# Kernel optimization log

Measured on AMD Instinct MI355X. Metric: run time of the kernel, lower is better.

Reference implementation:

```python
import jax, jax.numpy as jnp
import numpy as np

N_NODES = 500000
N_EDGES = 8000000
REPR_DIM = 32
TEMPO_DIM = 8
N_CLUSTERS = 5
NUM_NEG = 3
BATCH_SIZE = 100000  # multiple of NUM_NEG+2 = 5


def setup_inputs() -> dict:
    key = jax.random.key(0)
    ks = jax.random.split(key, 24)
    s = 0.05
    inp = {
        'x': jax.random.normal(ks[0], (N_NODES, 32), jnp.float32),
        'weight': jax.random.uniform(ks[1], (N_EDGES,), jnp.float32),
        # positional (repr) GraphSAGE params
        'e_w1l': jax.random.normal(ks[2], (32, REPR_DIM)) * s,
        'e_b1l': jax.random.normal(ks[3], (REPR_DIM,)) * s,
        'e_w1r': jax.random.normal(ks[4], (32 + REPR_DIM, REPR_DIM)) * s,
        'e_b1r': jax.random.normal(ks[5], (REPR_DIM,)) * s,
        'e_w2l': jax.random.normal(ks[6], (REPR_DIM, REPR_DIM)) * s,
        'e_b2l': jax.random.normal(ks[7], (REPR_DIM,)) * s,
        'e_w2r': jax.random.normal(ks[8], (2 * REPR_DIM, REPR_DIM)) * s,
        'e_b2r': jax.random.normal(ks[9], (REPR_DIM,)) * s,
        # temporal GraphSAGE params
        't_w1l': jax.random.normal(ks[10], (32, TEMPO_DIM)) * s,
        't_b1l': jax.random.normal(ks[11], (TEMPO_DIM,)) * s,
        't_w1r': jax.random.normal(ks[12], (32 + TEMPO_DIM, TEMPO_DIM)) * s,
        't_b1r': jax.random.normal(ks[13], (TEMPO_DIM,)) * s,
        't_w2l': jax.random.normal(ks[14], (TEMPO_DIM, TEMPO_DIM)) * s,
        't_b2l': jax.random.normal(ks[15], (TEMPO_DIM,)) * s,
        't_w2r': jax.random.normal(ks[16], (2 * TEMPO_DIM, TEMPO_DIM)) * s,
        't_b2r': jax.random.normal(ks[17], (TEMPO_DIM,)) * s,
        # centroid embeddings
        'cent': jax.random.normal(ks[18], (N_CLUSTERS, REPR_DIM)),
        'cent_t': jax.random.normal(ks[19], (N_CLUSTERS, TEMPO_DIM)),
        'edge_index': jax.random.randint(ks[20], (2, N_EDGES), 0, N_NODES, jnp.int32),
        'batch_size': BATCH_SIZE,
    }
    return inp


def _pinsage_layer(x, src, dst, w, Wl, bl, Wr, br):
    # z_n = relu(lin_l(x)); agg = weighted-mean of z_n over incoming edges
    n = x.shape[0]
    z = jax.nn.relu(x @ Wl + bl)                               # [N, d]
    agg_w = jax.ops.segment_sum(w, dst, num_segments=n) + 1.0  # [N]
    gathered = z[src] * w[:, None]                             # [E, d]
    agg = jax.ops.segment_sum(gathered, dst, num_segments=n) / agg_w[:, None]
    return jax.nn.relu(jnp.concatenate([x, agg], axis=1) @ Wr + br)


def _sage_module(x, src, dst, w, w1l, b1l, w1r, b1r, w2l, b2l, w2r, b2r, bs):
    h = _pinsage_layer(x, src, dst, w, w1l, b1l, w1r, b1r)
    h = jax.nn.relu(h)  # redundant (already relu'd) but matches source
    h = _pinsage_layer(h, src, dst, w, w2l, b2l, w2r, b2r)
    return h[:bs]


def reference(x, weight, e_w1l, e_b1l, e_w1r, e_b1r, e_w2l, e_b2l, e_w2r, e_b2r,
              t_w1l, t_b1l, t_w1r, t_b1r, t_w2l, t_b2l, t_w2r, t_b2r,
              cent, cent_t, edge_index, batch_size):
    src, dst = edge_index[0], edge_index[1]
    emb_posi = _sage_module(x, src, dst, weight, e_w1l, e_b1l, e_w1r, e_b1r,
                            e_w2l, e_b2l, e_w2r, e_b2r, batch_size)
    emb_temp = _sage_module(x, src, dst, weight, t_w1l, t_b1l, t_w1r, t_b1r,
                            t_w2l, t_b2l, t_w2r, t_b2r, batch_size)
    k = NUM_NEG + 2
    b = batch_size // k
    z = jnp.concatenate([emb_posi.reshape(b, k, REPR_DIM),
                         emb_temp.reshape(b, k, TEMPO_DIM)], axis=2)  # [B,5,40]
    ctr, pos, neg = z[:, 0], z[:, 1], z[:, 2:]
    pos_d = jnp.sum(ctr * pos, axis=-1)                                # [B]
    neg_d = jnp.max(jnp.einsum('bd,bkd->bk', ctr, neg), axis=1)        # [B]
    mm_loss = jnp.mean(jnp.maximum(neg_d - pos_d + 1.0, 0.0))
    # soft centroid assignment loss (optimize_comms=True path)
    C = jnp.concatenate([cent, cent_t], axis=1)                        # [K,40]
    q_ctr = jax.nn.softmax(ctr @ C.T, axis=-1)                         # [B,K]
    q_pos = jax.nn.softmax(pos @ C.T, axis=-1)                         # [B,K]
    q_neg = jax.nn.softmax(neg @ C.T, axis=-1)                         # [B,3,K]
    c_pos_d = jnp.sum(q_ctr * q_pos, axis=-1)
    c_neg_d = jnp.max(jnp.einsum('bc,bkc->bk', q_ctr, q_neg), axis=1)
    c_mm_loss = jnp.mean(jnp.maximum(c_neg_d - c_pos_d + 1.0, 0.0))
    q = jnp.concatenate([q_ctr[:, None], q_pos[:, None], q_neg], axis=1).reshape(-1, N_CLUSTERS)
    ne = jnp.mean(jnp.sum(q * jnp.log(q + 1e-20), axis=-1))  # negative entropy regularizer
    return mm_loss + c_mm_loss + ne * 0.01
```

## Files before the change

### kernel.cpp

```cpp
#include <hip/hip_runtime.h>

#define BS 100000
#define BQ 20000
#define NWG 512
#define CB  1024
#define NCMAX 512
#define CAP 17408

typedef unsigned long long ull;

__device__ __forceinline__ float relu_(float v) { return fmaxf(v, 0.0f); }

__device__ __forceinline__ unsigned enc12(float f) {
    unsigned u = __float_as_uint(f);
    if (u < 0x38000000u) return 0u;
    unsigned r = u - 0x38000000u;
    unsigned b = (r + 0x7FFFu + ((r >> 16) & 1u)) >> 16;
    return (b > 0xFFFu) ? 0xFFFu : b;
}
__device__ __forceinline__ float dec12(unsigned b) {
    return __uint_as_float((b << 16) + 0x38000000u);
}


__global__ __launch_bounds__(1024) void hist_kernel(
    const int* __restrict__ dst, int E, int NC, int per, int* __restrict__ hist2D)
{
    __shared__ int lc[NCMAX];
    int t = threadIdx.x, g = blockIdx.x;
    for (int i = t; i < NC; i += 1024) lc[i] = 0;
    __syncthreads();
    int lo = g * per, hi = min(lo + per, E);
    if (lo < hi) {
        int nq = (hi - lo) >> 2;
        const int4* dst4 = (const int4*)(dst + lo);
        for (int q = t; q < nq; q += 1024) {
            int4 d = dst4[q];
            atomicAdd(&lc[d.x >> 10], 1);
            atomicAdd(&lc[d.y >> 10], 1);
            atomicAdd(&lc[d.z >> 10], 1);
            atomicAdd(&lc[d.w >> 10], 1);
        }
        for (int i = lo + (nq << 2) + t; i < hi; i += 1024)
            atomicAdd(&lc[dst[i] >> 10], 1);
    }
    __syncthreads();
    for (int b = t; b < NC; b += 1024) hist2D[(size_t)b * NWG + g] = lc[b];
}

__global__ __launch_bounds__(256) void reduce_kernel(
    const int* __restrict__ hist2D, int* __restrict__ bucketTot)
{
    __shared__ int s[256];
    int b = blockIdx.x, t = threadIdx.x;
    int sum = 0;
    for (int g = t; g < NWG; g += 256) sum += hist2D[(size_t)b * NWG + g];
    s[t] = sum;
    __syncthreads();
    for (int d = 128; d > 0; d >>= 1) {
        if (t < d) s[t] += s[t + d];
        __syncthreads();
    }
    if (t == 0) bucketTot[b] = s[0];
}

__global__ __launch_bounds__(512) void scanTot_kernel(
    const int* __restrict__ bucketTot, int NC, int* __restrict__ bucketBase)
{
    __shared__ int s[512];
    int t = threadIdx.x;
    int v = (t < NC) ? bucketTot[t] : 0;
    s[t] = v;
    __syncthreads();
    for (int d = 1; d < 512; d <<= 1) {
        int x = (t >= d) ? s[t - d] : 0;
        __syncthreads();
        s[t] += x;
        __syncthreads();
    }
    if (t < NC) bucketBase[t] = s[t] - v;
}

__global__ __launch_bounds__(NWG) void scanB_kernel(
    const int* __restrict__ hist2D, const int* __restrict__ bucketBase,
    int* __restrict__ wgbase)
{
    __shared__ int s[NWG];
    int b = blockIdx.x, g = threadIdx.x;
    int v = hist2D[(size_t)b * NWG + g];
    s[g] = v;
    __syncthreads();
    for (int d = 1; d < NWG; d <<= 1) {
        int x = (g >= d) ? s[g - d] : 0;
        __syncthreads();
        s[g] += x;
        __syncthreads();
    }
    wgbase[(size_t)b * NWG + g] = bucketBase[b] + s[g] - v;
}

__device__ __forceinline__ void fillA_one(int d, int s, float wv,
    int* cur, ull* __restrict__ tmp)
{
    int b = d >> 10;
    int pos = atomicAdd(&cur[b], 1);
    ull rec = (ull)__float_as_uint(wv)
            | ((ull)(unsigned int)s << 32)
            | ((ull)(unsigned int)(d & (CB - 1)) << 51);
    tmp[pos] = rec;
}

__global__ __launch_bounds__(1024) void fillA_kernel(
    const int* __restrict__ src, const int* __restrict__ dst,
    const float* __restrict__ w, int E, int NC, int per,
    const int* __restrict__ wgbase, ull* __restrict__ tmp)
{
    __shared__ int cur[NCMAX];
    int t = threadIdx.x, g = blockIdx.x;
    for (int i = t; i < NC; i += 1024) cur[i] = wgbase[(size_t)i * NWG + g];
    __syncthreads();
    int lo = g * per, hi = min(lo + per, E);
    if (lo >= hi) return;
    int nq = (hi - lo) >> 2;
    const int4* src4 = (const int4*)(src + lo);
    const int4* dst4 = (const int4*)(dst + lo);
    const float4* w4 = (const float4*)(w + lo);
    for (int q = t; q < nq; q += 1024) {
        int4 d = dst4[q];
        int4 s = src4[q];
        float4 wv = w4[q];
        fillA_one(d.x, s.x, wv.x, cur, tmp);
        fillA_one(d.y, s.y, wv.y, cur, tmp);
        fillA_one(d.z, s.z, wv.z, cur, tmp);
        fillA_one(d.w, s.w, wv.w, cur, tmp);
    }
    for (int i = lo + (nq << 2) + t; i < hi; i += 1024)
        fillA_one(dst[i], src[i], w[i], cur, tmp);
}

__global__ __launch_bounds__(1024) void fillA2B_kernel(
    const ull* __restrict__ tmp, const int* __restrict__ wgbase,
    int NC, int N, int E,
    unsigned* __restrict__ csr, int* __restrict__ offsets)
{
    __shared__ int cnt[CB];
    __shared__ int ssum[1024];
    extern __shared__ unsigned recs[];
    int b = blockIdx.x, t = threadIdx.x;
    int lo = wgbase[(size_t)b * NWG];
    int hi = (b == NC - 1) ? E : wgbase[(size_t)(b + 1) * NWG];
    int M = hi - lo;

    cnt[t] = 0;
    __syncthreads();
    {
        int k = t;
        for (; k + 1024 < M; k += 2048) {
            ull r0 = tmp[lo + k];
            ull r1 = tmp[lo + k + 1024];
            atomicAdd(&cnt[(int)(r0 >> 51)], 1);
            atomicAdd(&cnt[(int)(r1 >> 51)], 1);
        }
        if (k < M) atomicAdd(&cnt[(int)(tmp[lo + k] >> 51)], 1);
    }
    __syncthreads();

    int v = cnt[t];
    ssum[t] = v;
    __syncthreads();
    for (int d = 1; d < 1024; d <<= 1) {
        int x = (t >= d) ? ssum[t - d] : 0;
        __syncthreads();
        ssum[t] += x;
        __syncthreads();
    }
    int excl = ssum[t] - v;

    int node = b * CB + t;
    if (node < N) offsets[node] = lo + excl;
    if (b == NC - 1 && t == 0) offsets[N] = E;
    __syncthreads();
    cnt[t] = excl;
    __syncthreads();

    if (M <= CAP) {
        for (int e = lo + t; e < hi; e += 1024) {
            ull rec = tmp[e];
            int dl = (int)(rec >> 51);
            int pos = atomicAdd(&cnt[dl], 1);
            float w = __uint_as_float((unsigned int)(rec & 0xFFFFFFFFull));
            unsigned wq = (unsigned)fmaf(w, 8191.0f, 0.5f);
            unsigned sidx = (unsigned)((rec >> 32) & 0x7FFFFull);
            recs[pos] = (sidx << 13) | wq;
        }
        __syncthreads();
        for (int i = t; i < M; i += 1024)
            csr[lo + i] = recs[i];
    } else {
        for (int e = lo + t; e < hi; e += 1024) {
            ull rec = tmp[e];
            int dl = (int)(rec >> 51);
            int pos = atomicAdd(&cnt[dl], 1);
            float w = __uint_as_float((unsigned int)(rec & 0xFFFFFFFFull));
            unsigned wq = (unsigned)fmaf(w, 8191.0f, 0.5f);
            unsigned sidx = (unsigned)((rec >> 32) & 0x7FFFFull);
            csr[lo + pos] = (sidx << 13) | wq;
        }
    }
}

__global__ __launch_bounds__(256) void z1_kernel(
    const float* __restrict__ in,
    const float* __restrict__ we, const float* __restrict__ be,
    const float* __restrict__ wt, const float* __restrict__ bt,
    unsigned* __restrict__ zq, int n)
{
    __shared__ float sWe[32 * 32];
    __shared__ float sWt[32 * 8];
    __shared__ float sBe[32];
    __shared__ float sBt[8];
    for (int i = threadIdx.x; i < 32 * 32; i += 256) sWe[i] = we[i];
    for (int i = threadIdx.x; i < 32 * 8; i += 256) sWt[i] = wt[i];
    if (threadIdx.x < 32) sBe[threadIdx.x] = be[threadIdx.x];
    if (threadIdx.x < 8)  sBt[threadIdx.x] = bt[threadIdx.x];
    __syncthreads();

    int node = blockIdx.x * 256 + threadIdx.x;
    if (node >= n) return;

    float row[32];
    {
        const float4* rp = (const float4*)(in + (size_t)node * 32);
        #pragma unroll
        for (int q = 0; q < 8; q++) {
            float4 v = rp[q];
            row[4*q] = v.x; row[4*q+1] = v.y; row[4*q+2] = v.z; row[4*q+3] = v.w;
        }
    }

    float o[40];
    #pragma unroll
    for (int j = 0; j < 32; j++) o[j] = sBe[j];
    #pragma unroll
    for (int i = 0; i < 32; i++) {
        float v = row[i];
        #pragma unroll
        for (int j = 0; j < 32; j++) o[j] = fmaf(v, sWe[i * 32 + j], o[j]);
    }
    #pragma unroll
    for (int j = 0; j < 8; j++) o[32 + j] = sBt[j];
    #pragma unroll
    for (int i = 0; i < 32; i++) {
        float v = row[i];
        #pragma unroll
        for (int j = 0; j < 8; j++) o[32 + j] = fmaf(v, sWt[i * 8 + j], o[32 + j]);
    }

    unsigned b[40];
    #pragma unroll
    for (int i = 0; i < 40; i++) b[i] = enc12(relu_(o[i]));
    unsigned wd[16];
    #pragma unroll
    for (int k = 0; k < 5; k++) {
        wd[3*k+0] = b[8*k+0] | (b[8*k+1] << 12) | (b[8*k+2] << 24);
        wd[3*k+1] = (b[8*k+2] >> 8) | (b[8*k+3] << 4) | (b[8*k+4] << 16) | (b[8*k+5] << 28);
        wd[3*k+2] = (b[8*k+5] >> 4) | (b[8*k+6] << 8) | (b[8*k+7] << 20);
    }
    wd[15] = 0;
    uint4* zv = (uint4*)(zq + (size_t)node * 16);
    #pragma unroll
    for (int q = 0; q < 4; q++)
        zv[q] = make_uint4(wd[4*q], wd[4*q+1], wd[4*q+2], wd[4*q+3]);
}

__device__ __forceinline__ void acc_edge(float* acc, float w,
    const uint4& A, const uint4& B, const uint4& C, const uint4& D)
{
    unsigned wds[15] = {A.x, A.y, A.z, A.w, B.x, B.y, B.z, B.w,
                        C.x, C.y, C.z, C.w, D.x, D.y, D.z};
    #pragma unroll
    for (int k = 0; k < 5; k++) {
        unsigned xw = wds[3*k+0], yw = wds[3*k+1], zw = wds[3*k+2];
        acc[8*k+0] = fmaf(w, dec12(xw & 0xFFFu),                       acc[8*k+0]);
        acc[8*k+1] = fmaf(w, dec12((xw >> 12) & 0xFFFu),               acc[8*k+1]);
        acc[8*k+2] = fmaf(w, dec12(((xw >> 24) | (yw << 8)) & 0xFFFu), acc[8*k+2]);
        acc[8*k+3] = fmaf(w, dec12((yw >> 4) & 0xFFFu),                acc[8*k+3]);
        acc[8*k+4] = fmaf(w, dec12((yw >> 16) & 0xFFFu),               acc[8*k+4]);
        acc[8*k+5] = fmaf(w, dec12(((yw >> 28) | (zw << 4)) & 0xFFFu), acc[8*k+5]);
        acc[8*k+6] = fmaf(w, dec12((zw >> 8) & 0xFFFu),                acc[8*k+6]);
        acc[8*k+7] = fmaf(w, dec12((zw >> 20) & 0xFFFu),               acc[8*k+7]);
    }
}

template <int RW, int TIN, int TOFF, bool EMITZ>
__global__ __launch_bounds__(256) void fin_kernel(
    const float* __restrict__ in,
    const unsigned* __restrict__ zq,
    const int* __restrict__ offsets,
    const unsigned* __restrict__ csr,
    const float* __restrict__ wre, const float* __restrict__ bre,
    const float* __restrict__ wrt, const float* __restrict__ brt,
    const float* __restrict__ w2e, const float* __restrict__ b2e,
    const float* __restrict__ w2t, const float* __restrict__ b2t,
    float* __restrict__ outbuf, int nOut,
    unsigned* __restrict__ zq2,
    int n)
{
    __shared__ float sWe[64 * 32];
    __shared__ float sWt[(TIN + 8) * 8];
    __shared__ float sBe[32];
    __shared__ float sBt[8];
    __shared__ float sW2e[32 * 32];
    __shared__ float sW2t[8 * 8];
    __shared__ float sB2e[32];
    __shared__ float sB2t[8];
    for (int i = threadIdx.x; i < 64 * 32; i += 256) sWe[i] = wre[i];
    for (int i = threadIdx.x; i < (TIN + 8) * 8; i += 256) sWt[i] = wrt[i];
    if (threadIdx.x < 32) sBe[threadIdx.x] = bre[threadIdx.x];
    if (threadIdx.x < 8)  sBt[threadIdx.x] = brt[threadIdx.x];
    if (EMITZ) {
        for (int i = threadIdx.x; i < 32 * 32; i += 256) sW2e[i] = w2e[i];
        for (int i = threadIdx.x; i < 8 * 8; i += 256) sW2t[i] = w2t[i];
        if (threadIdx.x < 32) sB2e[threadIdx.x] = b2e[threadIdx.x];
        if (threadIdx.x < 8)  sB2t[threadIdx.x] = b2t[threadIdx.x];
    }
    __syncthreads();

    int node = blockIdx.x * 256 + threadIdx.x;
    if (node >= n) return;

    float acc[40];
    #pragma unroll
    for (int j = 0; j < 40; j++) acc[j] = 0.0f;
    float wsum = 1.0f;

    const float DW = 1.0f / 8191.0f;
    int e0 = offsets[node];
    int e1 = offsets[node + 1];
    int e = e0;
    for (; e + 2 <= e1; e += 2) {
        unsigned pk0 = csr[e];
        unsigned pk1 = csr[e + 1];
        const uint4* p0 = (const uint4*)(zq + (size_t)(pk0 >> 13) * 16);
        const uint4* p1 = (const uint4*)(zq + (size_t)(pk1 >> 13) * 16);
        uint4 A0 = p0[0], B0 = p0[1], C0 = p0[2], D0 = p0[3];
        uint4 A1 = p1[0], B1 = p1[1], C1 = p1[2], D1 = p1[3];
        float w0 = (float)(pk0 & 8191u) * DW;
        float w1 = (float)(pk1 & 8191u) * DW;
        acc_edge(acc, w0, A0, B0, C0, D0);
        acc_edge(acc, w1, A1, B1, C1, D1);
        wsum += w0;
        wsum += w1;
    }
    if (e < e1) {
        unsigned pk = csr[e];
        const uint4* zp = (const uint4*)(zq + (size_t)(pk >> 13) * 16);
        uint4 A = zp[0], B = zp[1], C = zp[2], D = zp[3];
        float w = (float)(pk & 8191u) * DW;
        acc_edge(acc, w, A, B, C, D);
        wsum += w;
    }
    float inv = 1.0f / wsum;
    #pragma unroll
    for (int j = 0; j < 40; j++) acc[j] *= inv;

    float row[RW];
    {
        const float4* rp = (const float4*)(in + (size_t)node * RW);
        #pragma unroll
        for (int q = 0; q < RW / 4; q++) {
            float4 v = rp[q];
            row[4*q] = v.x; row[4*q+1] = v.y; row[4*q+2] = v.z; row[4*q+3] = v.w;
        }
    }

    float h[40];

    {
        float o[32];
        #pragma unroll
        for (int j = 0; j < 32; j++) o[j] = sBe[j];
        #pragma unroll
        for (int i = 0; i < 32; i++) {
            float v = row[i];
            #pragma unroll
            for (int j = 0; j < 32; j++) o[j] = fmaf(v, sWe[i * 32 + j], o[j]);
        }
        #pragma unroll
        for (int i = 0; i < 32; i++) {
            float v = acc[i];
            #pragma unroll
            for (int j = 0; j < 32; j++) o[j] = fmaf(v, sWe[(32 + i) * 32 + j], o[j]);
        }
        #pragma unroll
        for (int j = 0; j < 32; j++) h[j] = relu_(o[j]);
    }
    {
        float ot[8];
        #pragma unroll
        for (int j = 0; j < 8; j++) ot[j] = sBt[j];
        #pragma unroll
        for (int i = 0; i < TIN; i++) {
            float v = row[TOFF + i];
            #pragma unroll
            for (int j = 0; j < 8; j++) ot[j] = fmaf(v, sWt[i * 8 + j], ot[j]);
        }
        #pragma unroll
        for (int i = 0; i < 8; i++) {
            float v = acc[32 + i];
            #pragma unroll
            for (int j = 0; j < 8; j++) ot[j] = fmaf(v, sWt[(TIN + i) * 8 + j], ot[j]);
        }
        #pragma unroll
        for (int j = 0; j < 8; j++) h[32 + j] = relu_(ot[j]);
    }

    if (node < nOut) {
        float4* ov = (float4*)(outbuf + (size_t)node * 40);
        #pragma unroll
        for (int q = 0; q < 10; q++)
            ov[q] = make_float4(h[4*q], h[4*q+1], h[4*q+2], h[4*q+3]);
    }

    if (EMITZ) {
        float z2[40];
        #pragma unroll
        for (int j = 0; j < 32; j++) z2[j] = sB2e[j];
        #pragma unroll
        for (int i = 0; i < 32; i++) {
            float v = h[i];
            #pragma unroll
            for (int j = 0; j < 32; j++) z2[j] = fmaf(v, sW2e[i * 32 + j], z2[j]);
        }
        #pragma unroll
        for (int j = 0; j < 8; j++) z2[32 + j] = sB2t[j];
        #pragma unroll
        for (int i = 0; i < 8; i++) {
            float v = h[32 + i];
            #pragma unroll
            for (int j = 0; j < 8; j++) z2[32 + j] = fmaf(v, sW2t[i * 8 + j], z2[32 + j]);
        }
        unsigned b[40];
        #pragma unroll
        for (int i = 0; i < 40; i++) b[i] = enc12(relu_(z2[i]));
        unsigned wd[16];
        #pragma unroll
        for (int k = 0; k < 5; k++) {
            wd[3*k+0] = b[8*k+0] | (b[8*k+1] << 12) | (b[8*k+2] << 24);
            wd[3*k+1] = (b[8*k+2] >> 8) | (b[8*k+3] << 4) | (b[8*k+4] << 16) | (b[8*k+5] << 28);
            wd[3*k+2] = (b[8*k+5] >> 4) | (b[8*k+6] << 8) | (b[8*k+7] << 20);
        }
        wd[15] = 0;
        uint4* zv = (uint4*)(zq2 + (size_t)node * 16);
        #pragma unroll
        for (int q = 0; q < 4; q++)
            zv[q] = make_uint4(wd[4*q], wd[4*q+1], wd[4*q+2], wd[4*q+3]);
    }
}


__device__ __forceinline__ void load40(const float* p, float* r) {
    const float4* v = (const float4*)p;
    #pragma unroll
    for (int q = 0; q < 10; q++) {
        float4 t = v[q];
        r[4*q] = t.x; r[4*q+1] = t.y; r[4*q+2] = t.z; r[4*q+3] = t.w;
    }
}

__device__ __forceinline__ float dot40(const float* a, const float* b) {
    float s = 0.0f;
    #pragma unroll
    for (int d = 0; d < 40; d++) s = fmaf(a[d], b[d], s);
    return s;
}

__device__ __forceinline__ void softmax5(const float l[5], float q[5]) {
    float m = l[0];
    #pragma unroll
    for (int c = 1; c < 5; c++) m = fmaxf(m, l[c]);
    float s = 0.0f;
    #pragma unroll
    for (int c = 0; c < 5; c++) { q[c] = expf(l[c] - m); s += q[c]; }
    float inv = 1.0f / s;
    #pragma unroll
    for (int c = 0; c < 5; c++) q[c] *= inv;
}

__device__ __forceinline__ float ent5(const float q[5]) {
    float e = 0.0f;
    #pragma unroll
    for (int c = 0; c < 5; c++) e += q[c] * logf(q[c] + 1e-20f);
    return e;
}

__device__ __forceinline__ float dot5(const float* a, const float* b) {
    float s = 0.0f;
    #pragma unroll
    for (int c = 0; c < 5; c++) s += a[c] * b[c];
    return s;
}

__global__ __launch_bounds__(256) void loss_kernel(
    const float* __restrict__ emb,
    const float* __restrict__ cent,
    const float* __restrict__ cent_t,
    float* __restrict__ out)
{
    __shared__ float sC[5 * 40];
    for (int i = threadIdx.x; i < 200; i += 256) {
        int c = i / 40, d = i % 40;
        sC[i] = (d < 32) ? cent[c * 32 + d] : cent_t[c * 8 + (d - 32)];
    }
    __syncthreads();

    int i = blockIdx.x * 256 + threadIdx.x;
    float contrib = 0.0f;
    if (i < BQ) {
        const float* base = emb + (size_t)i * 200;

        float ctr[40];
        load40(base, ctr);
        float l[5];
        #pragma unroll
        for (int c = 0; c < 5; c++) l[c] = dot40(ctr, sC + c * 40);
        float qc[5];
        softmax5(l, qc);
        float ent = ent5(qc);

        float rowv[40];
        load40(base + 40, rowv);
        float pd = dot40(ctr, rowv);
        #pragma unroll
        for (int c = 0; c < 5; c++) l[c] = dot40(rowv, sC + c * 40);
        float qp[5];
        softmax5(l, qp);
        float cpd = dot5(qc, qp);
        ent += ent5(qp);

        float nd = -1e30f, cnd = -1e30f;
        #pragma unroll
        for (int k = 0; k < 3; k++) {
            load40(base + (2 + k) * 40, rowv);
            nd = fmaxf(nd, dot40(ctr, rowv));
            #pragma unroll
            for (int c = 0; c < 5; c++) l[c] = dot40(rowv, sC + c * 40);
            float qn[5];
            softmax5(l, qn);
            cnd = fmaxf(cnd, dot5(qc, qn));
            ent += ent5(qn);
        }

        float mm  = fmaxf(nd - pd + 1.0f, 0.0f);
        float cmm = fmaxf(cnd - cpd + 1.0f, 0.0f);
        contrib = (mm + cmm) * (1.0f / (float)BQ) + 0.01f * (1.0f / (float)BS) * ent;
    }

    #pragma unroll
    for (int off = 32; off > 0; off >>= 1) contrib += __shfl_down(contrib, off);
    if ((threadIdx.x & 63) == 0) atomicAdd(out, contrib);
}


extern "C" void kernel_launch(void* const* d_in, const int* in_sizes, int n_in,
                              void* d_out, int out_size, void* d_ws, size_t ws_size,
                              hipStream_t stream) {
    const float* x      = (const float*)d_in[0];
    const float* weight = (const float*)d_in[1];
    const float* e_w1l  = (const float*)d_in[2];
    const float* e_b1l  = (const float*)d_in[3];
    const float* e_w1r  = (const float*)d_in[4];
    const float* e_b1r  = (const float*)d_in[5];
    const float* e_w2l  = (const float*)d_in[6];
    const float* e_b2l  = (const float*)d_in[7];
    const float* e_w2r  = (const float*)d_in[8];
    const float* e_b2r  = (const float*)d_in[9];
    const float* t_w1l  = (const float*)d_in[10];
    const float* t_b1l  = (const float*)d_in[11];
    const float* t_w1r  = (const float*)d_in[12];
    const float* t_b1r  = (const float*)d_in[13];
    const float* t_w2l  = (const float*)d_in[14];
    const float* t_b2l  = (const float*)d_in[15];
    const float* t_w2r  = (const float*)d_in[16];
    const float* t_b2r  = (const float*)d_in[17];
    const float* cent   = (const float*)d_in[18];
    const float* cent_t = (const float*)d_in[19];
    const int*   eidx   = (const int*)d_in[20];

    const int E = in_sizes[20] / 2;
    const int N = in_sizes[0] / 32;
    const int* srcI = eidx;
    const int* dstI = eidx + E;
    float* out = (float*)d_out;

    const int NC = (N + CB - 1) / CB;
    const int per = (((E + NWG - 1) / NWG) + 3) & ~3;

    char* p = (char*)d_ws;
    auto alloc = [&](size_t bytes) -> char* {
        char* r = p;
        p += (bytes + 255) & ~(size_t)255;
        return r;
    };
    char* regionA = alloc((size_t)E * 8);
    ull*  tmp     = (ull*)regionA;
    unsigned* zq1 = (unsigned*)regionA;
    unsigned* zq2 = (unsigned*)alloc((size_t)N * 64);
    float* hcat   = (float*)alloc((size_t)BS * 40 * 4);
    float* emb    = (float*)alloc((size_t)BS * 40 * 4);
    unsigned* csr = (unsigned*)alloc((size_t)E * 4);
    int*   offsets= (int*)alloc((size_t)(N + 1) * 4);
    int*   hist2D = (int*)alloc((size_t)NC * NWG * 4);
    int*   wgbase = (int*)alloc((size_t)NC * NWG * 4);
    int*   bucketTot  = (int*)alloc((size_t)NC * 4);
    int*   bucketBase = (int*)alloc((size_t)NC * 4);
    (void)ws_size;

    hipMemsetAsync(d_out, 0, sizeof(float), stream);

    hist_kernel<<<NWG, 1024, 0, stream>>>(dstI, E, NC, per, hist2D);
    reduce_kernel<<<NC, 256, 0, stream>>>(hist2D, bucketTot);
    scanTot_kernel<<<1, 512, 0, stream>>>(bucketTot, NC, bucketBase);
    scanB_kernel<<<NC, NWG, 0, stream>>>(hist2D, bucketBase, wgbase);
    fillA_kernel<<<NWG, 1024, 0, stream>>>(srcI, dstI, weight, E, NC, per, wgbase, tmp);
    fillA2B_kernel<<<NC, 1024, (size_t)CAP * 4, stream>>>(tmp, wgbase, NC, N, E, csr, offsets);

    const int nb = (N + 255) / 256;
    z1_kernel<<<nb, 256, 0, stream>>>(x, e_w1l, e_b1l, t_w1l, t_b1l, zq1, N);
    fin_kernel<32, 32, 0, true><<<nb, 256, 0, stream>>>(
        x, zq1, offsets, csr,
        e_w1r, e_b1r, t_w1r, t_b1r,
        e_w2l, e_b2l, t_w2l, t_b2l,
        hcat, BS, zq2, N);
    const int nb2 = (BS + 255) / 256;
    fin_kernel<40, 8, 32, false><<<nb2, 256, 0, stream>>>(
        hcat, zq2, offsets, csr,
        e_w2r, e_b2r, t_w2r, t_b2r,
        nullptr, nullptr, nullptr, nullptr,
        emb, BS, nullptr, BS);

    loss_kernel<<<(BQ + 255) / 256, 256, 0, stream>>>(emb, cent, cent_t, out);
}
```

Measured before the change: 506.5 us.

## Stage fillA scatter writes in LDS ring buffers and flush full cache lines

The bucket-scatter pass now stages records in a per-bucket shared-memory ring and flushes completed 8-record (64-byte) lines to global memory as whole lines, instead of writing each 8-byte record to a random address. To keep those lines aligned, each workgroup's per-bucket segment is padded to a multiple of 8. Records carry a valid bit, and the later CSR pass skips padding entries. Two separate bucket scans are kept, one padded and one actual, so CSR offsets stay compact. The trade-off is extra block-wide barriers and flush loops per edge step, a slightly larger temporary buffer, and padded reads in the second pass.

After: 462.6 us. 8.7% less time.

```diff
diff --git a/kernel.cpp b/kernel.cpp
--- a/kernel.cpp
+++ b/kernel.cpp
@@ -6,6 +6,7 @@
 #define CB  1024
 #define NCMAX 512
 #define CAP 17408
+#define RING_D 16
 
 typedef unsigned long long ull;
 
@@ -49,27 +50,34 @@
 }
 
 __global__ __launch_bounds__(256) void reduce_kernel(
-    const int* __restrict__ hist2D, int* __restrict__ bucketTot)
-{
-    __shared__ int s[256];
+    const int* __restrict__ hist2D, int* __restrict__ bucketTotPad,
+    int* __restrict__ bucketTotAct)
+{
+    __shared__ int sp[256];
+    __shared__ int sa[256];
     int b = blockIdx.x, t = threadIdx.x;
-    int sum = 0;
-    for (int g = t; g < NWG; g += 256) sum += hist2D[(size_t)b * NWG + g];
-    s[t] = sum;
+    int sumP = 0, sumA = 0;
+    for (int g = t; g < NWG; g += 256) {
+        int c = hist2D[(size_t)b * NWG + g];
+        sumA += c;
+        sumP += (c + 7) & ~7;
+    }
+    sp[t] = sumP; sa[t] = sumA;
     __syncthreads();
     for (int d = 128; d > 0; d >>= 1) {
-        if (t < d) s[t] += s[t + d];
-        __syncthreads();
-    }
-    if (t == 0) bucketTot[b] = s[0];
+        if (t < d) { sp[t] += sp[t + d]; sa[t] += sa[t + d]; }
+        __syncthreads();
+    }
+    if (t == 0) { bucketTotPad[b] = sp[0]; bucketTotAct[b] = sa[0]; }
 }
 
 __global__ __launch_bounds__(512) void scanTot_kernel(
-    const int* __restrict__ bucketTot, int NC, int* __restrict__ bucketBase)
+    const int* __restrict__ bucketTotPad, const int* __restrict__ bucketTotAct,
+    int NC, int* __restrict__ bucketBasePad, int* __restrict__ bucketBaseAct)
 {
     __shared__ int s[512];
     int t = threadIdx.x;
-    int v = (t < NC) ? bucketTot[t] : 0;
+    int v = (t < NC) ? bucketTotPad[t] : 0;
     s[t] = v;
     __syncthreads();
     for (int d = 1; d < 512; d <<= 1) {
@@ -78,16 +86,28 @@
         s[t] += x;
         __syncthreads();
     }
-    if (t < NC) bucketBase[t] = s[t] - v;
+    if (t < NC) bucketBasePad[t] = s[t] - v;
+    if (t == NC - 1) bucketBasePad[NC] = s[t];
+    __syncthreads();
+    int va = (t < NC) ? bucketTotAct[t] : 0;
+    s[t] = va;
+    __syncthreads();
+    for (int d = 1; d < 512; d <<= 1) {
+        int x = (t >= d) ? s[t - d] : 0;
+        __syncthreads();
+        s[t] += x;
+        __syncthreads();
+    }
+    if (t < NC) bucketBaseAct[t] = s[t] - va;
 }
 
 __global__ __launch_bounds__(NWG) void scanB_kernel(
-    const int* __restrict__ hist2D, const int* __restrict__ bucketBase,
+    const int* __restrict__ hist2D, const int* __restrict__ bucketBasePad,
     int* __restrict__ wgbase)
 {
     __shared__ int s[NWG];
     int b = blockIdx.x, g = threadIdx.x;
-    int v = hist2D[(size_t)b * NWG + g];
+    int v = (hist2D[(size_t)b * NWG + g] + 7) & ~7;
     s[g] = v;
     __syncthreads();
     for (int d = 1; d < NWG; d <<= 1) {
@@ -96,18 +116,7 @@
         s[g] += x;
         __syncthreads();
     }
-    wgbase[(size_t)b * NWG + g] = bucketBase[b] + s[g] - v;
-}
-
-__device__ __forceinline__ void fillA_one(int d, int s, float wv,
-    int* cur, ull* __restrict__ tmp)
-{
-    int b = d >> 10;
-    int pos = atomicAdd(&cur[b], 1);
-    ull rec = (ull)__float_as_uint(wv)
-            | ((ull)(unsigned int)s << 32)
-            | ((ull)(unsigned int)(d & (CB - 1)) << 51);
-    tmp[pos] = rec;
+    wgbase[(size_t)b * NWG + g] = bucketBasePad[b] + s[g] - v;
 }
 
 __global__ __launch_bounds__(1024) void fillA_kernel(
@@ -115,31 +124,122 @@
     const float* __restrict__ w, int E, int NC, int per,
     const int* __restrict__ wgbase, ull* __restrict__ tmp)
 {
+    extern __shared__ ull ring[];
     __shared__ int cur[NCMAX];
+    __shared__ int flq[NCMAX];
+    __shared__ unsigned vmask[NCMAX];
     int t = threadIdx.x, g = blockIdx.x;
-    for (int i = t; i < NC; i += 1024) cur[i] = wgbase[(size_t)i * NWG + g];
-    __syncthreads();
+    for (int i = t; i < NC; i += 1024) {
+        int base = wgbase[(size_t)i * NWG + g];
+        cur[i] = base;
+        flq[i] = base >> 3;
+        vmask[i] = 0u;
+    }
+    __syncthreads();
+
     int lo = g * per, hi = min(lo + per, E);
-    if (lo >= hi) return;
-    int nq = (hi - lo) >> 2;
-    const int4* src4 = (const int4*)(src + lo);
-    const int4* dst4 = (const int4*)(dst + lo);
-    const float4* w4 = (const float4*)(w + lo);
-    for (int q = t; q < nq; q += 1024) {
-        int4 d = dst4[q];
-        int4 s = src4[q];
-        float4 wv = w4[q];
-        fillA_one(d.x, s.x, wv.x, cur, tmp);
-        fillA_one(d.y, s.y, wv.y, cur, tmp);
-        fillA_one(d.z, s.z, wv.z, cur, tmp);
-        fillA_one(d.w, s.w, wv.w, cur, tmp);
-    }
-    for (int i = lo + (nq << 2) + t; i < hi; i += 1024)
-        fillA_one(dst[i], src[i], w[i], cur, tmp);
+    int groups = (per + 4095) >> 12;
+    for (int gi = 0; gi < groups; gi++) {
+        int eb = lo + (gi << 12) + (t << 2);
+        int4 d4 = make_int4(0, 0, 0, 0), s4 = make_int4(0, 0, 0, 0);
+        float4 w4 = make_float4(0, 0, 0, 0);
+        if (eb + 4 <= hi) {
+            d4 = *(const int4*)(dst + eb);
+            s4 = *(const int4*)(src + eb);
+            w4 = *(const float4*)(w + eb);
+        } else if (eb < hi) {
+            int m = hi - eb;
+            if (m > 0) { d4.x = dst[eb];     s4.x = src[eb];     w4.x = w[eb]; }
+            if (m > 1) { d4.y = dst[eb + 1]; s4.y = src[eb + 1]; w4.y = w[eb + 1]; }
+            if (m > 2) { d4.z = dst[eb + 2]; s4.z = src[eb + 2]; w4.z = w[eb + 2]; }
+        }
+        #pragma unroll
+        for (int k = 0; k < 4; k++) {
+            if (eb + k < hi) {
+                int d = (k == 0) ? d4.x : (k == 1) ? d4.y : (k == 2) ? d4.z : d4.w;
+                int s = (k == 0) ? s4.x : (k == 1) ? s4.y : (k == 2) ? s4.z : s4.w;
+                float wv = (k == 0) ? w4.x : (k == 1) ? w4.y : (k == 2) ? w4.z : w4.w;
+                int b = d >> 10;
+                ull rec = (1ull << 63)
+                        | ((ull)(unsigned)(d & (CB - 1)) << 51)
+                        | ((ull)(unsigned)s << 32)
+                        | (ull)__float_as_uint(wv);
+                int pos = atomicAdd(&cur[b], 1);
+                if ((pos >> 3) < flq[b] + 2) {
+                    int slot = pos & 15;
+                    ring[b * RING_D + slot] = rec;
+                    atomicOr(&vmask[b], 1u << slot);
+                } else {
+                    tmp[pos] = rec;
+                }
+            }
+            __syncthreads();
+            if (t < NC) {
+                int bb = t;
+                int endL = cur[bb] >> 3;
+                int L = flq[bb];
+                unsigned vm = vmask[bb];
+                while (L < endL) {
+                    int half = (L & 1) << 3;
+                    unsigned m8 = (vm >> half) & 0xFFu;
+                    ull* dp = tmp + ((size_t)L << 3);
+                    const ull* rp = ring + bb * RING_D + half;
+                    if (m8 == 0xFFu) {
+                        uint4* d16 = (uint4*)dp;
+                        const uint4* r16 = (const uint4*)rp;
+                        d16[0] = r16[0]; d16[1] = r16[1];
+                        d16[2] = r16[2]; d16[3] = r16[3];
+                    } else if (m8) {
+                        #pragma unroll
+                        for (int j = 0; j < 8; j++)
+                            if (m8 & (1u << j)) dp[j] = rp[j];
+                    }
+                    vm &= ~(0xFFu << half);
+                    L++;
+                }
+                vmask[bb] = vm;
+                flq[bb] = L;
+            }
+            __syncthreads();
+        }
+    }
+
+    if (t < NC) {
+        int bb = t;
+        int c = cur[bb];
+        int padded = (c + 7) & ~7;
+        unsigned vm = vmask[bb];
+        for (int p = c; p < padded; p++) {
+            int slot = p & 15;
+            ring[bb * RING_D + slot] = 0ull;
+            vm |= 1u << slot;
+        }
+        int endL = padded >> 3;
+        int L = flq[bb];
+        while (L < endL) {
+            int half = (L & 1) << 3;
+            unsigned m8 = (vm >> half) & 0xFFu;
+            ull* dp = tmp + ((size_t)L << 3);
+            const ull* rp = ring + bb * RING_D + half;
+            if (m8 == 0xFFu) {
+                uint4* d16 = (uint4*)dp;
+                const uint4* r16 = (const uint4*)rp;
+                d16[0] = r16[0]; d16[1] = r16[1];
+                d16[2] = r16[2]; d16[3] = r16[3];
+            } else if (m8) {
+                #pragma unroll
+                for (int j = 0; j < 8; j++)
+                    if (m8 & (1u << j)) dp[j] = rp[j];
+            }
+            vm &= ~(0xFFu << half);
+            L++;
+        }
+    }
 }
 
 __global__ __launch_bounds__(1024) void fillA2B_kernel(
     const ull* __restrict__ tmp, const int* __restrict__ wgbase,
+    const int* __restrict__ bucketBasePad, const int* __restrict__ bucketBaseAct,
     int NC, int N, int E,
     unsigned* __restrict__ csr, int* __restrict__ offsets)
 {
@@ -148,20 +248,14 @@
     extern __shared__ unsigned recs[];
     int b = blockIdx.x, t = threadIdx.x;
     int lo = wgbase[(size_t)b * NWG];
-    int hi = (b == NC - 1) ? E : wgbase[(size_t)(b + 1) * NWG];
-    int M = hi - lo;
+    int hi = (b == NC - 1) ? bucketBasePad[NC] : wgbase[(size_t)(b + 1) * NWG];
+    int actLo = bucketBaseAct[b];
 
     cnt[t] = 0;
     __syncthreads();
-    {
-        int k = t;
-        for (; k + 1024 < M; k += 2048) {
-            ull r0 = tmp[lo + k];
-            ull r1 = tmp[lo + k + 1024];
-            atomicAdd(&cnt[(int)(r0 >> 51)], 1);
-            atomicAdd(&cnt[(int)(r1 >> 51)], 1);
-        }
-        if (k < M) atomicAdd(&cnt[(int)(tmp[lo + k] >> 51)], 1);
+    for (int e = lo + t; e < hi; e += 1024) {
+        ull rec = tmp[e];
+        if (rec >> 63) atomicAdd(&cnt[(int)((rec >> 51) & (CB - 1))], 1);
     }
     __syncthreads();
 
@@ -175,18 +269,20 @@
         __syncthreads();
     }
     int excl = ssum[t] - v;
+    int Mact = ssum[1023];
 
     int node = b * CB + t;
-    if (node < N) offsets[node] = lo + excl;
+    if (node < N) offsets[node] = actLo + excl;
     if (b == NC - 1 && t == 0) offsets[N] = E;
     __syncthreads();
     cnt[t] = excl;
     __syncthreads();
 
-    if (M <= CAP) {
+    if (Mact <= CAP) {
         for (int e = lo + t; e < hi; e += 1024) {
             ull rec = tmp[e];
-            int dl = (int)(rec >> 51);
+            if (!(rec >> 63)) continue;
+            int dl = (int)((rec >> 51) & (CB - 1));
             int pos = atomicAdd(&cnt[dl], 1);
             float w = __uint_as_float((unsigned int)(rec & 0xFFFFFFFFull));
             unsigned wq = (unsigned)fmaf(w, 8191.0f, 0.5f);
@@ -194,17 +290,18 @@
             recs[pos] = (sidx << 13) | wq;
         }
         __syncthreads();
-        for (int i = t; i < M; i += 1024)
-            csr[lo + i] = recs[i];
+        for (int i = t; i < Mact; i += 1024)
+            csr[actLo + i] = recs[i];
     } else {
         for (int e = lo + t; e < hi; e += 1024) {
             ull rec = tmp[e];
-            int dl = (int)(rec >> 51);
+            if (!(rec >> 63)) continue;
+            int dl = (int)((rec >> 51) & (CB - 1));
             int pos = atomicAdd(&cnt[dl], 1);
             float w = __uint_as_float((unsigned int)(rec & 0xFFFFFFFFull));
             unsigned wq = (unsigned)fmaf(w, 8191.0f, 0.5f);
             unsigned sidx = (unsigned)((rec >> 32) & 0x7FFFFull);
-            csr[lo + pos] = (sidx << 13) | wq;
+            csr[actLo + pos] = (sidx << 13) | wq;
         }
     }
 }
@@ -595,6 +692,7 @@
 
     const int NC = (N + CB - 1) / CB;
     const int per = (((E + NWG - 1) / NWG) + 3) & ~3;
+    const size_t tmpRecs = (size_t)E + (size_t)NC * NWG * 8;
 
     char* p = (char*)d_ws;
     auto alloc = [&](size_t bytes) -> char* {
@@ -602,7 +700,7 @@
         p += (bytes + 255) & ~(size_t)255;
         return r;
     };
-    char* regionA = alloc((size_t)E * 8);
+    char* regionA = alloc(tmpRecs * 8);
     ull*  tmp     = (ull*)regionA;
     unsigned* zq1 = (unsigned*)regionA;
     unsigned* zq2 = (unsigned*)alloc((size_t)N * 64);
@@ -612,18 +710,23 @@
     int*   offsets= (int*)alloc((size_t)(N + 1) * 4);
     int*   hist2D = (int*)alloc((size_t)NC * NWG * 4);
     int*   wgbase = (int*)alloc((size_t)NC * NWG * 4);
-    int*   bucketTot  = (int*)alloc((size_t)NC * 4);
-    int*   bucketBase = (int*)alloc((size_t)NC * 4);
+    int*   bucketTotPad  = (int*)alloc((size_t)NC * 4);
+    int*   bucketTotAct  = (int*)alloc((size_t)NC * 4);
+    int*   bucketBasePad = (int*)alloc((size_t)(NC + 1) * 4);
+    int*   bucketBaseAct = (int*)alloc((size_t)NC * 4);
     (void)ws_size;
 
     hipMemsetAsync(d_out, 0, sizeof(float), stream);
 
     hist_kernel<<<NWG, 1024, 0, stream>>>(dstI, E, NC, per, hist2D);
-    reduce_kernel<<<NC, 256, 0, stream>>>(hist2D, bucketTot);
-    scanTot_kernel<<<1, 512, 0, stream>>>(bucketTot, NC, bucketBase);
-    scanB_kernel<<<NC, NWG, 0, stream>>>(hist2D, bucketBase, wgbase);
-    fillA_kernel<<<NWG, 1024, 0, stream>>>(srcI, dstI, weight, E, NC, per, wgbase, tmp);
-    fillA2B_kernel<<<NC, 1024, (size_t)CAP * 4, stream>>>(tmp, wgbase, NC, N, E, csr, offsets);
+    reduce_kernel<<<NC, 256, 0, stream>>>(hist2D, bucketTotPad, bucketTotAct);
+    scanTot_kernel<<<1, 512, 0, stream>>>(bucketTotPad, bucketTotAct, NC,
+                                          bucketBasePad, bucketBaseAct);
+    scanB_kernel<<<NC, NWG, 0, stream>>>(hist2D, bucketBasePad, wgbase);
+    fillA_kernel<<<NWG, 1024, (size_t)NC * RING_D * 8, stream>>>(
+        srcI, dstI, weight, E, NC, per, wgbase, tmp);
+    fillA2B_kernel<<<NC, 1024, (size_t)CAP * 4, stream>>>(
+        tmp, wgbase, bucketBasePad, bucketBaseAct, NC, N, E, csr, offsets);
 
     const int nb = (N + 255) / 256;
     z1_kernel<<<nb, 256, 0, stream>>>(x, e_w1l, e_b1l, t_w1l, t_b1l, zq1, N);
```
